# Kernel tuning notes

Measured on AMD Instinct MI355X. Metric: run time of the kernel, lower is better.

## Reference

```python
import jax, jax.numpy as jnp
import numpy as np

KEEPRATE = 0.5


def setup_inputs() -> dict:
    key = jax.random.key(0)
    k1, k2, k3 = jax.random.split(key, 3)
    N, C, T, V, K = 64, 128, 256, 25, 3
    x = jax.random.normal(k1, (N, C, T, V), dtype=jnp.float32)
    A = jax.random.uniform(k2, (N, K, V, V), dtype=jnp.float32)
    p = jax.random.normal(k3, (C * T, 1), dtype=jnp.float32)
    return {"x": x, "A": A, "p": p}


def reference(x, A, p):
    N, C, T, V = x.shape
    Vk = int(KEEPRATE * V)  # number of joints kept
    # [N, V, C*T]
    xr = jnp.transpose(x.reshape(N, C * T, V), (0, 2, 1))
    # l2-normalized projection vector, score per node
    pn = p * jax.lax.rsqrt(jnp.sum(p * p))
    y = xr @ pn                       # [N, V, 1]
    ys = y[..., 0]                    # [N, V]
    idx = jnp.argsort(-ys, axis=-1)[:, :Vk]   # [N, Vk] top-k node indices
    y_hat = jax.nn.sigmoid(jnp.take_along_axis(ys, idx, axis=1))[..., None]  # [N, Vk, 1]
    xg = jnp.take_along_axis(xr, idx[..., None], axis=1) * y_hat             # [N, Vk, C*T]
    # adjacency squaring then row+col gather of kept nodes
    A2 = A @ A                        # [N, K, V, V]

    def _sel(a2, i):                  # a2: [K, V, V], i: [Vk]
        return a2[:, i][:, :, i]      # [K, Vk, Vk]

    A_out = jax.vmap(_sel)(A2, idx)   # [N, K, Vk, Vk]
    x_out = jnp.transpose(xg, (0, 2, 1)).reshape(N, C, T, Vk)
    return x_out, A_out
```

## Files before the change

kernel.cpp:

```cpp
#include <hip/hip_runtime.h>
#include <hip/hip_bf16.h>
#include <math.h>

constexpr int N  = 64;
constexpr int V  = 25;
constexpr int K  = 3;
constexpr int CT = 32768;
constexpr int VK = 12;
constexpr int SPLIT = 32;
constexpr int ROWS  = 256;
constexpr int NBLK_G = N * (CT / ROWS);


__device__ __forceinline__ void gload_lds16(const float* g, float* l) {
    __builtin_amdgcn_global_load_lds(
        (const __attribute__((address_space(1))) void*)g,
        (__attribute__((address_space(3))) void*)l, 16, 0, 0);
}

__device__ __forceinline__ void stage_wave(const float* __restrict__ gsrc, float* lds,
                                           int wave, int lane) {
    const float* gw = gsrc + (size_t)wave * 1600;
    float* lw = lds + wave * 1600;
    #pragma unroll
    for (int i = 0; i < 6; ++i)
        gload_lds16(gw + (size_t)(i * 64 + lane) * 4, lw + i * 256);
    if (lane < 16)
        gload_lds16(gw + (size_t)(384 + lane) * 4, lw + 384 * 4);
}

__global__ __launch_bounds__(256) void k_scores(const float* __restrict__ x,
                                                const float* __restrict__ p,
                                                float* __restrict__ partial_t,
                                                float* __restrict__ p2partial) {
    const int n = blockIdx.x / SPLIT;
    const int s = blockIdx.x % SPLIT;
    constexpr int CHUNK = CT / SPLIT;
    constexpr int TILES = CHUNK / ROWS;
    const int ct0 = s * CHUNK;
    const float* xn = x + (size_t)n * CT * V;
    const int tid = threadIdx.x, wave = tid >> 6, lane = tid & 63;

    __shared__ float lds[ROWS * V];

    float acc[V];
    #pragma unroll
    for (int v = 0; v < V; ++v) acc[v] = 0.f;
    float psq = 0.f;

    for (int tile = 0; tile < TILES; ++tile) {
        const int base_ct = ct0 + tile * ROWS;
        asm volatile("s_waitcnt lgkmcnt(0)" ::: "memory");
        stage_wave(xn + (size_t)base_ct * V, lds, wave, lane);
        asm volatile("s_waitcnt vmcnt(0)" ::: "memory");

        const float pv = p[base_ct + tid];
        psq += pv * pv;
        const float* row = lds + tid * V;
        #pragma unroll
        for (int v = 0; v < V; ++v) acc[v] += row[v] * pv;
    }

    #pragma unroll
    for (int v = 0; v < V; ++v) {
        float a = acc[v];
        #pragma unroll
        for (int off = 32; off > 0; off >>= 1) a += __shfl_down(a, off);
        acc[v] = a;
    }
    #pragma unroll
    for (int off = 32; off > 0; off >>= 1) psq += __shfl_down(psq, off);

    __shared__ float red[4][V];
    __shared__ float redp[4];
    if (lane == 0) {
        #pragma unroll
        for (int v = 0; v < V; ++v) red[wave][v] = acc[v];
        redp[wave] = psq;
    }
    __syncthreads();
    if (tid < V) {
        partial_t[((size_t)n * V + tid) * SPLIT + s] =
            red[0][tid] + red[1][tid] + red[2][tid] + red[3][tid];
    }
    if (tid == V && n == 0) {
        p2partial[s] = redp[0] + redp[1] + redp[2] + redp[3];
    }
}

__device__ __forceinline__ void wave_topk(const float* __restrict__ partial_t,
                                          const float* __restrict__ p2partial,
                                          int n, int lane, int* swidx, float* swyh) {
    float s2 = 0.f;
    #pragma unroll
    for (int i = 0; i < SPLIT; ++i) s2 += p2partial[i];

    float my = 0.f;
    if (lane < V) {
        const float4* pb = (const float4*)(partial_t + ((size_t)n * V + lane) * SPLIT);
        #pragma unroll
        for (int i = 0; i < SPLIT / 4; ++i) {
            float4 q = pb[i];
            my += q.x + q.y + q.z + q.w;
        }
    }
    int rank = 0;
    #pragma unroll
    for (int u = 0; u < V; ++u) {
        const float yu = __shfl(my, u);
        if (yu > my || (yu == my && u < lane)) ++rank;
    }
    if (lane < V && rank < VK) {
        swidx[rank] = lane;
        swyh[rank]  = 1.0f / (1.0f + expf(-my * rsqrtf(s2)));
    }
}

__global__ __launch_bounds__(256) void k_gather_aout(const float* __restrict__ x,
                                                     const float* __restrict__ A,
                                                     const float* __restrict__ partial_t,
                                                     const float* __restrict__ p2partial,
                                                     float* __restrict__ xout,
                                                     float* __restrict__ aout) {
    __shared__ float lds[ROWS * V];
    __shared__ int   swidx[4][VK];
    __shared__ float swyh[4][VK];
    const int tid = threadIdx.x, wave = tid >> 6, lane = tid & 63;

    if (blockIdx.x < (unsigned)NBLK_G) {
        const int n  = blockIdx.x >> 7;
        const int r0 = (blockIdx.x & 127) << 8;

        stage_wave(x + ((size_t)n * CT + r0) * V, lds, wave, lane);
        wave_topk(partial_t, p2partial, n, lane, swidx[wave], swyh[wave]);
        asm volatile("s_waitcnt vmcnt(0) lgkmcnt(0)" ::: "memory");

        float4* dst = (float4*)(xout + ((size_t)n * CT + r0) * VK);
        #pragma unroll
        for (int j = 0; j < 3; ++j) {
            const int f   = 192 * wave + 64 * j + lane;
            const int row = f / 3;
            const int c0  = (f % 3) * 4;
            float4 o;
            o.x = lds[row * V + swidx[wave][c0 + 0]] * swyh[wave][c0 + 0];
            o.y = lds[row * V + swidx[wave][c0 + 1]] * swyh[wave][c0 + 1];
            o.z = lds[row * V + swidx[wave][c0 + 2]] * swyh[wave][c0 + 2];
            o.w = lds[row * V + swidx[wave][c0 + 3]] * swyh[wave][c0 + 3];
            dst[f] = o;
        }
    } else {
        if (wave != 0) return;
        const int b2 = blockIdx.x - NBLK_G;
        const int n  = b2 / K;
        const int k  = b2 % K;
        wave_topk(partial_t, p2partial, n, lane, swidx[0], swyh[0]);
        const float* Ak = A + ((size_t)n * K + k) * V * V;
        for (int i = lane; i < V * V; i += 64) lds[i] = Ak[i];
        asm volatile("s_waitcnt vmcnt(0) lgkmcnt(0)" ::: "memory");
        for (int o = lane; o < VK * VK; o += 64) {
            const int a  = o / VK, bc = o % VK;
            const int ia = swidx[0][a], ib = swidx[0][bc];
            float ssum = 0.f;
            #pragma unroll
            for (int m = 0; m < V; ++m) ssum += lds[ia * V + m] * lds[m * V + ib];
            aout[((size_t)n * K + k) * VK * VK + o] = ssum;
        }
    }
}

extern "C" void kernel_launch(void* const* d_in, const int* in_sizes, int n_in,
                              void* d_out, int out_size, void* d_ws, size_t ws_size,
                              hipStream_t stream) {
    const float* x = (const float*)d_in[0];
    const float* A = (const float*)d_in[1];
    const float* p = (const float*)d_in[2];

    float* xout = (float*)d_out;
    float* aout = xout + (size_t)N * CT * VK;

    char* ws = (char*)d_ws;
    float* partial_t = (float*)(ws);
    float* p2partial = (float*)(ws + 204800);

    k_scores<<<N * SPLIT, 256, 0, stream>>>(x, p, partial_t, p2partial);
    k_gather_aout<<<NBLK_G + N * K, 256, 0, stream>>>(x, A, partial_t, p2partial, xout, aout);
}
```

Baseline: 94.20 us.

## Double-buffer score staging, split top-k into own kernel, use nontemporal stores

The score kernel now double-buffers LDS tiles, prefetches all p values up front, and uses partial vmcnt waits so the next tile's global-to-LDS load overlaps the current tile's dot products. Top-k selection moves out of every gather block into a small separate kernel that writes indices and sigmoid weights to workspace, and gather blocks just load them. Output writes use nontemporal stores. The trade is an extra kernel launch and more LDS per scores block, which may reduce occupancy.

```diff
diff --git a/kernel.cpp b/kernel.cpp
--- a/kernel.cpp
+++ b/kernel.cpp
@@ -9,7 +9,11 @@
 constexpr int VK = 12;
 constexpr int SPLIT = 32;
 constexpr int ROWS  = 256;
+constexpr int CHUNK = CT / SPLIT;
+constexpr int TILES = CHUNK / ROWS;
 constexpr int NBLK_G = N * (CT / ROWS);
+
+typedef float f32x4 __attribute__((ext_vector_type(4)));
 
 
 __device__ __forceinline__ void gload_lds16(const float* g, float* l) {
@@ -18,10 +22,10 @@
         (__attribute__((address_space(3))) void*)l, 16, 0, 0);
 }
 
-__device__ __forceinline__ void stage_wave(const float* __restrict__ gsrc, float* lds,
+__device__ __forceinline__ void stage_wave(const float* __restrict__ gsrc, float* ldsbuf,
                                            int wave, int lane) {
     const float* gw = gsrc + (size_t)wave * 1600;
-    float* lw = lds + wave * 1600;
+    float* lw = ldsbuf + wave * 1600;
     #pragma unroll
     for (int i = 0; i < 6; ++i)
         gload_lds16(gw + (size_t)(i * 64 + lane) * 4, lw + i * 256);
@@ -35,30 +39,39 @@
                                                 float* __restrict__ p2partial) {
     const int n = blockIdx.x / SPLIT;
     const int s = blockIdx.x % SPLIT;
-    constexpr int CHUNK = CT / SPLIT;
-    constexpr int TILES = CHUNK / ROWS;
     const int ct0 = s * CHUNK;
     const float* xn = x + (size_t)n * CT * V;
     const int tid = threadIdx.x, wave = tid >> 6, lane = tid & 63;
 
-    __shared__ float lds[ROWS * V];
+    __shared__ float lds[2][ROWS * V];
+
+    float pv[TILES];
+    #pragma unroll
+    for (int t = 0; t < TILES; ++t) pv[t] = p[ct0 + t * ROWS + tid];
+
+    stage_wave(xn + (size_t)(ct0 + 0 * ROWS) * V, lds[0], wave, lane);
+    stage_wave(xn + (size_t)(ct0 + 1 * ROWS) * V, lds[1], wave, lane);
 
     float acc[V];
     #pragma unroll
     for (int v = 0; v < V; ++v) acc[v] = 0.f;
     float psq = 0.f;
 
-    for (int tile = 0; tile < TILES; ++tile) {
-        const int base_ct = ct0 + tile * ROWS;
-        asm volatile("s_waitcnt lgkmcnt(0)" ::: "memory");
-        stage_wave(xn + (size_t)base_ct * V, lds, wave, lane);
-        asm volatile("s_waitcnt vmcnt(0)" ::: "memory");
-
-        const float pv = p[base_ct + tid];
-        psq += pv * pv;
-        const float* row = lds + tid * V;
-        #pragma unroll
-        for (int v = 0; v < V; ++v) acc[v] += row[v] * pv;
+    #pragma unroll
+    for (int t = 0; t < TILES; ++t) {
+        if (t < TILES - 1) asm volatile("s_waitcnt vmcnt(7)" ::: "memory");
+        else               asm volatile("s_waitcnt vmcnt(0)" ::: "memory");
+
+        const float pvt = pv[t];
+        psq += pvt * pvt;
+        const float* row = lds[t & 1] + tid * V;
+        #pragma unroll
+        for (int v = 0; v < V; ++v) acc[v] += row[v] * pvt;
+
+        if (t + 2 < TILES) {
+            asm volatile("s_waitcnt lgkmcnt(0)" ::: "memory");
+            stage_wave(xn + (size_t)(ct0 + (t + 2) * ROWS) * V, lds[t & 1], wave, lane);
+        }
     }
 
     #pragma unroll
@@ -88,9 +101,11 @@
     }
 }
 
-__device__ __forceinline__ void wave_topk(const float* __restrict__ partial_t,
-                                          const float* __restrict__ p2partial,
-                                          int n, int lane, int* swidx, float* swyh) {
+__global__ __launch_bounds__(64) void k_topk(const float* __restrict__ partial_t,
+                                             const float* __restrict__ p2partial,
+                                             int* __restrict__ idxbuf,
+                                             float* __restrict__ yhatbuf) {
+    const int n = blockIdx.x, lane = threadIdx.x;
     float s2 = 0.f;
     #pragma unroll
     for (int i = 0; i < SPLIT; ++i) s2 += p2partial[i];
@@ -111,15 +126,15 @@
         if (yu > my || (yu == my && u < lane)) ++rank;
     }
     if (lane < V && rank < VK) {
-        swidx[rank] = lane;
-        swyh[rank]  = 1.0f / (1.0f + expf(-my * rsqrtf(s2)));
+        idxbuf[n * VK + rank]  = lane;
+        yhatbuf[n * VK + rank] = 1.0f / (1.0f + expf(-my * rsqrtf(s2)));
     }
 }
 
 __global__ __launch_bounds__(256) void k_gather_aout(const float* __restrict__ x,
                                                      const float* __restrict__ A,
-                                                     const float* __restrict__ partial_t,
-                                                     const float* __restrict__ p2partial,
+                                                     const int* __restrict__ idxbuf,
+                                                     const float* __restrict__ yhatbuf,
                                                      float* __restrict__ xout,
                                                      float* __restrict__ aout) {
     __shared__ float lds[ROWS * V];
@@ -132,28 +147,31 @@
         const int r0 = (blockIdx.x & 127) << 8;
 
         stage_wave(x + ((size_t)n * CT + r0) * V, lds, wave, lane);
-        wave_topk(partial_t, p2partial, n, lane, swidx[wave], swyh[wave]);
+        if (lane < VK) {
+            swidx[wave][lane] = idxbuf[n * VK + lane];
+            swyh[wave][lane]  = yhatbuf[n * VK + lane];
+        }
         asm volatile("s_waitcnt vmcnt(0) lgkmcnt(0)" ::: "memory");
 
-        float4* dst = (float4*)(xout + ((size_t)n * CT + r0) * VK);
+        f32x4* dst = (f32x4*)(xout + ((size_t)n * CT + r0) * VK);
         #pragma unroll
         for (int j = 0; j < 3; ++j) {
             const int f   = 192 * wave + 64 * j + lane;
             const int row = f / 3;
             const int c0  = (f % 3) * 4;
-            float4 o;
+            f32x4 o;
             o.x = lds[row * V + swidx[wave][c0 + 0]] * swyh[wave][c0 + 0];
             o.y = lds[row * V + swidx[wave][c0 + 1]] * swyh[wave][c0 + 1];
             o.z = lds[row * V + swidx[wave][c0 + 2]] * swyh[wave][c0 + 2];
             o.w = lds[row * V + swidx[wave][c0 + 3]] * swyh[wave][c0 + 3];
-            dst[f] = o;
+            __builtin_nontemporal_store(o, &dst[f]);
         }
     } else {
         if (wave != 0) return;
         const int b2 = blockIdx.x - NBLK_G;
         const int n  = b2 / K;
         const int k  = b2 % K;
-        wave_topk(partial_t, p2partial, n, lane, swidx[0], swyh[0]);
+        if (lane < VK) swidx[0][lane] = idxbuf[n * VK + lane];
         const float* Ak = A + ((size_t)n * K + k) * V * V;
         for (int i = lane; i < V * V; i += 64) lds[i] = Ak[i];
         asm volatile("s_waitcnt vmcnt(0) lgkmcnt(0)" ::: "memory");
@@ -163,7 +181,7 @@
             float ssum = 0.f;
             #pragma unroll
             for (int m = 0; m < V; ++m) ssum += lds[ia * V + m] * lds[m * V + ib];
-            aout[((size_t)n * K + k) * VK * VK + o] = ssum;
+            __builtin_nontemporal_store(ssum, &aout[((size_t)n * K + k) * VK * VK + o]);
         }
     }
 }
@@ -181,7 +199,10 @@
     char* ws = (char*)d_ws;
     float* partial_t = (float*)(ws);
     float* p2partial = (float*)(ws + 204800);
+    float* yhatbuf   = (float*)(ws + 204928);
+    int*   idxbuf    = (int*)  (ws + 208000);
 
     k_scores<<<N * SPLIT, 256, 0, stream>>>(x, p, partial_t, p2partial);
-    k_gather_aout<<<NBLK_G + N * K, 256, 0, stream>>>(x, A, partial_t, p2partial, xout, aout);
-}
+    k_topk<<<N, 64, 0, stream>>>(partial_t, p2partial, idxbuf, yhatbuf);
+    k_gather_aout<<<NBLK_G + N * K, 256, 0, stream>>>(x, A, idxbuf, yhatbuf, xout, aout);
+}
```

Result: faster. 89.02 us, median of 2 (-5.5%).
